# Optimization experiments

Hardware: AMD Instinct MI355X
Metric: run time of the kernel (lower is better)

The kernel has to match this reference:

```python
import jax, jax.numpy as jnp
import numpy as np

N = 50000      # nodes
E = 800000     # edges (before self-loops)
IN = 128
OUT = 128
HID = 2 * OUT  # hi=2 in the module
NEG_SLOPE = 0.2


def setup_inputs() -> dict:
    key = jax.random.key(0)
    ks = jax.random.split(key, 12)
    glorot = lambda k, shape: jax.random.normal(k, shape, jnp.float32) * (2.0 / (shape[0] + shape[-1])) ** 0.5
    return {
        "x": jax.random.normal(ks[0], (N, IN), jnp.float32),
        "edge_index": jax.random.randint(ks[1], (2, E), 0, N, jnp.int64),
        # layer 1: in -> 2*out
        "W1": glorot(ks[2], (IN, HID)),
        "a1_src": glorot(ks[3], (HID,)),
        "a1_dst": glorot(ks[4], (HID,)),
        "b1": jnp.zeros((HID,), jnp.float32),
        # layer 2: 2*out -> out
        "W2": glorot(ks[5], (HID, OUT)),
        "a2_src": glorot(ks[6], (OUT,)),
        "a2_dst": glorot(ks[7], (OUT,)),
        "b2": jnp.zeros((OUT,), jnp.float32),
    }


def gat_layer(x, src, dst, W, a_src, a_dst, b, n):
    # h = W x   [N, F]
    h = x @ W
    alpha_src = h @ a_src  # [N]
    alpha_dst = h @ a_dst  # [N]
    # per-edge attention logit, edge j->i uses src score of j + dst score of i
    e = jax.nn.leaky_relu(alpha_src[src] + alpha_dst[dst], NEG_SLOPE)  # [E']
    # numerically stable segment softmax over incoming edges of each dst node
    e_max = jax.lax.stop_gradient(jax.ops.segment_max(e, dst, num_segments=n))
    p = jnp.exp(e - e_max[dst])
    denom = jax.ops.segment_sum(p, dst, num_segments=n)
    alpha = p / (denom[dst] + 1e-16)  # [E']
    # weighted scatter-aggregate of source features
    out = jax.ops.segment_sum(h[src] * alpha[:, None], dst, num_segments=n)
    return out + b


def reference(x, edge_index, W1, a1_src, a1_dst, b1, W2, a2_src, a2_dst, b2):
    n = x.shape[0]
    loops = jnp.arange(n, dtype=edge_index.dtype)
    src = jnp.concatenate([edge_index[0], loops])  # add self-loops (PyG default)
    dst = jnp.concatenate([edge_index[1], loops])
    h = jax.nn.relu(gat_layer(x, src, dst, W1, a1_src, a1_dst, b1, n))
    out = jax.nn.relu(gat_layer(h, src, dst, W2, a2_src, a2_dst, b2, n))
    return out
```

## Files before the change

### kernel.cpp

```cpp
#include <hip/hip_runtime.h>
#include <hip/hip_bf16.h>
#include <float.h>
#include <stdint.h>

#define NEG_SLOPE 0.2f

typedef __attribute__((ext_vector_type(8))) short short8;
typedef __attribute__((ext_vector_type(4))) float f32x4;

#define BSTRIDE 3072

__device__ inline float b2f(unsigned short u) {
  return __uint_as_float((unsigned int)u << 16);
}
__device__ inline unsigned short f2b(float f) {
  unsigned int u = __float_as_uint(f);
  return (unsigned short)((u + 0x7FFF + ((u >> 16) & 1)) >> 16);
}
__device__ inline float leaky(float e) { return e >= 0.f ? e : NEG_SLOPE * e; }
__device__ inline float blo(unsigned int w) {
  return __uint_as_float(w << 16);
}
__device__ inline float bhi(unsigned int w) {
  return __uint_as_float(w & 0xFFFF0000u);
}

__global__ void detect_idx64_kernel(const void* ei, int* flag) {
  const int* p = (const int*)ei;
  int lane = threadIdx.x & 63;
  unsigned long long b = __ballot(p[2 * lane + 1] != 0);
  if (threadIdx.x == 0) *flag = (b == 0ull) ? 1 : 0;
}

__device__ inline int load_idx(const void* ei, long long pos, int is64) {
  if (is64) return (int)((const long long*)ei)[pos];
  return ((const int*)ei)[pos];
}

__global__ __launch_bounds__(256) void bin_edges(
    const void* __restrict__ ei, const int* __restrict__ flag64, int E,
    int* __restrict__ bcursor, unsigned int* __restrict__ binned) {
  __shared__ int hist[512];
  __shared__ int scn[512];
  __shared__ int gb[512];
  __shared__ unsigned int stage[2048];
  int t = threadIdx.x;
  hist[t] = 0; hist[t + 256] = 0;
  __syncthreads();
  const int is64 = *flag64;
  const long long base = (long long)blockIdx.x * 2048;
  const int cblk = (int)min((long long)2048, (long long)E - base);
  int sv[8];
  short bk[8], rk[8];
#pragma unroll
  for (int i = 0; i < 8; ++i) {
    int k = t + i * 256;
    if (k < cblk) {
      long long j = base + k;
      int s = load_idx(ei, j, is64);
      int d = load_idx(ei, (long long)E + j, is64);
      int b = d >> 7;
      bk[i] = (short)b;
      sv[i] = (s << 7) | (d & 127);
      rk[i] = (short)atomicAdd(&hist[b], 1);
    } else {
      bk[i] = -1;
    }
  }
  __syncthreads();
  scn[t] = hist[t]; scn[t + 256] = hist[t + 256];
  __syncthreads();
  for (int off = 1; off < 512; off <<= 1) {
    int v0 = (t >= off) ? scn[t - off] : 0;
    int v1 = scn[t + 256 - off];
    __syncthreads();
    scn[t] += v0;
    scn[t + 256] += v1;
    __syncthreads();
  }
  int c0 = hist[t], c1 = hist[t + 256];
  int l0 = scn[t] - c0, l1 = scn[t + 256] - c1;
  if (c0) gb[t] = atomicAdd(&bcursor[t], c0);
  if (c1) gb[t + 256] = atomicAdd(&bcursor[t + 256], c1);
  scn[t] = l0; scn[t + 256] = l1;
  __syncthreads();
#pragma unroll
  for (int i = 0; i < 8; ++i) {
    if (bk[i] >= 0)
      stage[scn[bk[i]] + rk[i]] = ((unsigned)(int)bk[i] << 23) | (unsigned)sv[i];
  }
  __syncthreads();
#pragma unroll
  for (int i = 0; i < 8; ++i) {
    int k = t + i * 256;
    if (k < cblk) {
      unsigned w = stage[k];
      int b = w >> 23;
      binned[(long long)b * BSTRIDE + gb[b] + (k - scn[b])] = w;
    }
  }
}

__global__ __launch_bounds__(256) void place_csr(
    const unsigned int* __restrict__ binned, const int* __restrict__ bcursor,
    int2* __restrict__ rowbe, unsigned short* __restrict__ csr, int Nn) {
  __shared__ int cnt[128], deg0[128], cur[128];
  int t = threadIdx.x;
  int b = blockIdx.x;
  if (t < 128) cnt[t] = 0;
  __syncthreads();
  const int rbeg = b * BSTRIDE;
  const int rend = rbeg + bcursor[b];
  for (int k = rbeg + t; k < rend; k += 256)
    atomicAdd(&cnt[binned[k] & 127], 1);
  __syncthreads();
  if (t < 128) deg0[t] = cnt[t];
  __syncthreads();
  for (int off = 1; off < 128; off <<= 1) {
    int v = (t >= off && t < 128) ? cnt[t - off] : 0;
    __syncthreads();
    if (t < 128) cnt[t] += v;
    __syncthreads();
  }
  const int node0 = b << 7;
  if (t < 128) {
    int start = rbeg + cnt[t] - deg0[t];
    int node = node0 + t;
    if (node < Nn) rowbe[node] = make_int2(start, start + deg0[t]);
    cur[t] = start;
  }
  __syncthreads();
  for (int k = rbeg + t; k < rend; k += 256) {
    unsigned w = binned[k];
    int pos = atomicAdd(&cur[w & 127], 1);
    csr[pos] = (unsigned short)((w >> 7) & 0xFFFF);
  }
}

__global__ __launch_bounds__(256) void prep_weights(
    const float* __restrict__ W1, const float* __restrict__ W2,
    const float* __restrict__ a1s, const float* __restrict__ a1d,
    const float* __restrict__ a2s, const float* __restrict__ a2d,
    unsigned short* __restrict__ Wp1, unsigned short* __restrict__ Wp2,
    float* __restrict__ wa) {
  int b = blockIdx.x;
  int t = threadIdx.x;
  if (b < 128) {
    int i = b * 256 + t;
    int k = i >> 8, n = i & 255;
    Wp1[(((k >> 3) * 256 + n) << 3) + (k & 7)] = f2b(W1[i]);
  } else if (b < 256) {
    int i = (b - 128) * 256 + t;
    int k = i >> 7, n = i & 127;
    Wp2[(((k >> 3) * 128 + n) << 3) + (k & 7)] = f2b(W2[i]);
  } else {
    int o = (b - 256) * 256 + t;
    float s = 0.f;
    if (o < 128) {
      for (int n = 0; n < 256; ++n) s += W1[o * 256 + n] * a1s[n];
    } else if (o < 256) {
      int k = o - 128;
      for (int n = 0; n < 256; ++n) s += W1[k * 256 + n] * a1d[n];
    } else if (o < 512) {
      int k = o - 256;
      for (int n = 0; n < 128; ++n) s += W2[k * 128 + n] * a2s[n];
    } else {
      int k = o - 512;
      for (int n = 0; n < 128; ++n) s += W2[k * 128 + n] * a2d[n];
    }
    wa[o] = s;
  }
}

__global__ __launch_bounds__(256) void alpha1_cast(
    const float* __restrict__ x, const float* __restrict__ wa,
    unsigned short* __restrict__ xb, float* __restrict__ as_out,
    float* __restrict__ ad_out, int Nn) {
  int node = blockIdx.x * 4 + (threadIdx.x >> 6);
  int lane = threadIdx.x & 63;
  if (node >= Nn) return;
  float2 v = *(const float2*)(x + (long long)node * 128 + lane * 2);
  float s1 = v.x * wa[lane * 2] + v.y * wa[lane * 2 + 1];
  float s2 = v.x * wa[128 + lane * 2] + v.y * wa[128 + lane * 2 + 1];
  unsigned int packed = (unsigned int)f2b(v.x) | ((unsigned int)f2b(v.y) << 16);
  *(unsigned int*)(xb + (long long)node * 128 + lane * 2) = packed;
#pragma unroll
  for (int off = 32; off > 0; off >>= 1) {
    s1 += __shfl_down(s1, off);
    s2 += __shfl_down(s2, off);
  }
  if (lane == 0) {
    as_out[node] = s1;
    ad_out[node] = s2;
  }
}

template <int Nn, int Kk, bool BIAS_RELU, bool SCORES>
__global__ __launch_bounds__(256) void gemm_mfma(
    const unsigned short* __restrict__ A, const unsigned short* __restrict__ Bp,
    unsigned short* __restrict__ C, int M, const float* __restrict__ bias,
    const float* __restrict__ was, const float* __restrict__ wad,
    float* __restrict__ s_as, float* __restrict__ s_ad) {
  const int l = threadIdx.x & 63;
  const int wm = threadIdx.x >> 6;
  const int bm = blockIdx.x * 64;
  const int bn = blockIdx.y * 64;
  const int arow = bm + wm * 16 + (l & 15);
  const int kg = l >> 4;

  f32x4 acc[4];
#pragma unroll
  for (int nt = 0; nt < 4; ++nt) acc[nt] = (f32x4){0.f, 0.f, 0.f, 0.f};

  const bool arow_ok = (arow < M);
  const bool do_scores = SCORES && (blockIdx.y == 0);
  float ps = 0.f, pd = 0.f;
#pragma unroll
  for (int kk = 0; kk < Kk; kk += 32) {
    short8 afrag;
    if (arow_ok)
      afrag = *(const short8*)(A + (long long)arow * Kk + kk + kg * 8);
    else
      afrag = (short8){0, 0, 0, 0, 0, 0, 0, 0};
    if (SCORES) {
      if (do_scores) {
        const int kb0 = kk + kg * 8;
#pragma unroll
        for (int i = 0; i < 8; ++i) {
          float v = b2f((unsigned short)afrag[i]);
          ps += v * was[kb0 + i];
          pd += v * wad[kb0 + i];
        }
      }
    }
    const int kb = (kk >> 3) + kg;
#pragma unroll
    for (int nt = 0; nt < 4; ++nt) {
      short8 bfrag = *(const short8*)(Bp + (((long long)kb * Nn + bn + nt * 16 +
                                             (l & 15))
                                            << 3));
      acc[nt] = __builtin_amdgcn_mfma_f32_16x16x32_bf16(afrag, bfrag, acc[nt],
                                                        0, 0, 0);
    }
  }
  if (SCORES) {
    if (do_scores) {
      ps += __shfl_xor(ps, 16); ps += __shfl_xor(ps, 32);
      pd += __shfl_xor(pd, 16); pd += __shfl_xor(pd, 32);
      if (l < 16 && arow_ok) {
        s_as[arow] = ps;
        s_ad[arow] = pd;
      }
    }
  }
#pragma unroll
  for (int nt = 0; nt < 4; ++nt) {
    const int col = bn + nt * 16 + (l & 15);
    float bv = BIAS_RELU ? bias[col] : 0.f;
#pragma unroll
    for (int r = 0; r < 4; ++r) {
      const int row = bm + wm * 16 + (l >> 4) * 4 + r;
      if (row < M) {
        float v = acc[nt][r];
        if (BIAS_RELU) v = fmaxf(v + bv, 0.f);
        C[(long long)row * Nn + col] = f2b(v);
      }
    }
  }
}

template <bool BIAS_RELU, bool OUT_BF16>
__global__ __launch_bounds__(256) void gat_aggregate(
    const int2* __restrict__ rowbe, const unsigned short* __restrict__ csr,
    const float* __restrict__ as, const float* __restrict__ ad,
    const unsigned short* __restrict__ h, const float* __restrict__ bias,
    void* __restrict__ outp, int Nn) {
  constexpr int F = 128;
  int node = blockIdx.x * 4 + (threadIdx.x >> 6);
  int lane = threadIdx.x & 63;
  if (node >= Nn) return;
  const int2 be = rowbe[node];
  const int beg = be.x, end = be.y;
  const int deg = end - beg;
  const float adn = ad[node];
  const int grp = lane >> 4;
  const int hl = lane & 15;
  const int f0 = hl * 8;

  const int chunk = (deg + 3) >> 2;
  int t = beg + grp * chunk;
  const int gend = min(t + chunk, end);

  float m, sg;
  float acc[8];
  if (grp == 0) {
    m = leaky(as[node] + adn);
    sg = 1.f;
    uint4 w = *(const uint4*)(h + (long long)node * F + f0);
    acc[0] = blo(w.x); acc[1] = bhi(w.x);
    acc[2] = blo(w.y); acc[3] = bhi(w.y);
    acc[4] = blo(w.z); acc[5] = bhi(w.z);
    acc[6] = blo(w.w); acc[7] = bhi(w.w);
  } else {
    m = -3.4e38f;
    sg = 0.f;
#pragma unroll
    for (int j = 0; j < 8; ++j) acc[j] = 0.f;
  }

  for (; t + 4 <= gend; t += 4) {
    int s0 = csr[t], s1 = csr[t + 1], s2 = csr[t + 2], s3 = csr[t + 3];
    uint4 w0 = *(const uint4*)(h + (long long)s0 * F + f0);
    uint4 w1 = *(const uint4*)(h + (long long)s1 * F + f0);
    uint4 w2 = *(const uint4*)(h + (long long)s2 * F + f0);
    uint4 w3 = *(const uint4*)(h + (long long)s3 * F + f0);
    float e0 = leaky(as[s0] + adn);
    float e1 = leaky(as[s1] + adn);
    float e2 = leaky(as[s2] + adn);
    float e3 = leaky(as[s3] + adn);
    float em = fmaxf(fmaxf(e0, e1), fmaxf(e2, e3));
    if (em > m + 8.f) {
      float sc = __expf(m - em);
      sg *= sc;
#pragma unroll
      for (int j = 0; j < 8; ++j) acc[j] *= sc;
      m = em;
    }
    float p0 = __expf(e0 - m), p1 = __expf(e1 - m);
    float p2 = __expf(e2 - m), p3 = __expf(e3 - m);
    sg += (p0 + p1) + (p2 + p3);
    acc[0] += p0 * blo(w0.x) + p1 * blo(w1.x) + p2 * blo(w2.x) + p3 * blo(w3.x);
    acc[1] += p0 * bhi(w0.x) + p1 * bhi(w1.x) + p2 * bhi(w2.x) + p3 * bhi(w3.x);
    acc[2] += p0 * blo(w0.y) + p1 * blo(w1.y) + p2 * blo(w2.y) + p3 * blo(w3.y);
    acc[3] += p0 * bhi(w0.y) + p1 * bhi(w1.y) + p2 * bhi(w2.y) + p3 * bhi(w3.y);
    acc[4] += p0 * blo(w0.z) + p1 * blo(w1.z) + p2 * blo(w2.z) + p3 * blo(w3.z);
    acc[5] += p0 * bhi(w0.z) + p1 * bhi(w1.z) + p2 * bhi(w2.z) + p3 * bhi(w3.z);
    acc[6] += p0 * blo(w0.w) + p1 * blo(w1.w) + p2 * blo(w2.w) + p3 * blo(w3.w);
    acc[7] += p0 * bhi(w0.w) + p1 * bhi(w1.w) + p2 * bhi(w2.w) + p3 * bhi(w3.w);
  }
  for (; t < gend; ++t) {
    int s = csr[t];
    uint4 w = *(const uint4*)(h + (long long)s * F + f0);
    float e = leaky(as[s] + adn);
    if (e > m + 8.f) {
      float sc = __expf(m - e);
      sg *= sc;
#pragma unroll
      for (int j = 0; j < 8; ++j) acc[j] *= sc;
      m = e;
    }
    float p = __expf(e - m);
    sg += p;
    acc[0] += p * blo(w.x); acc[1] += p * bhi(w.x);
    acc[2] += p * blo(w.y); acc[3] += p * bhi(w.y);
    acc[4] += p * blo(w.z); acc[5] += p * bhi(w.z);
    acc[6] += p * blo(w.w); acc[7] += p * bhi(w.w);
  }

#pragma unroll
  for (int off = 16; off <= 32; off <<= 1) {
    float mo = __shfl_xor(m, off);
    float so = __shfl_xor(sg, off);
    float mn = fmaxf(m, mo);
    float c0 = __expf(m - mn);
    float c1 = __expf(mo - mn);
    sg = sg * c0 + so * c1;
#pragma unroll
    for (int j = 0; j < 8; ++j) {
      float ao = __shfl_xor(acc[j], off);
      acc[j] = acc[j] * c0 + ao * c1;
    }
    m = mn;
  }
  const float inv = 1.f / (sg + 1e-16f);

  if (lane < 16) {
#pragma unroll
    for (int j = 0; j < 8; ++j) {
      acc[j] *= inv;
      if (BIAS_RELU) acc[j] = fmaxf(acc[j] + bias[f0 + j], 0.f);
    }
    if (OUT_BF16) {
      short8 o;
#pragma unroll
      for (int j = 0; j < 8; ++j) o[j] = (short)f2b(acc[j]);
      *(short8*)((unsigned short*)outp + (long long)node * F + f0) = o;
    } else {
      float4 o0 = {acc[0], acc[1], acc[2], acc[3]};
      float4 o1 = {acc[4], acc[5], acc[6], acc[7]};
      float* orow = (float*)outp + (long long)node * F + f0;
      *(float4*)(orow) = o0;
      *(float4*)(orow + 4) = o1;
    }
  }
}

extern "C" void kernel_launch(void* const* d_in, const int* in_sizes, int n_in,
                              void* d_out, int out_size, void* d_ws,
                              size_t ws_size, hipStream_t stream) {
  const float* x      = (const float*)d_in[0];
  const void*  ei     = d_in[1];
  const float* W1     = (const float*)d_in[2];
  const float* a1_src = (const float*)d_in[3];
  const float* a1_dst = (const float*)d_in[4];
  const float* b1     = (const float*)d_in[5];
  const float* W2     = (const float*)d_in[6];
  const float* a2_src = (const float*)d_in[7];
  const float* a2_dst = (const float*)d_in[8];
  const float* b2     = (const float*)d_in[9];
  float* out = (float*)d_out;

  const int N = 50000, E = 800000, IN = 128, HID = 256, OUT = 128;
  const int NBLK_E = (E + 2047) / 2048;
  const int NB = (N + 127) >> 7;

  char* ws = (char*)d_ws;
  size_t off = 0;
  auto carve = [&](size_t bytes) -> void* {
    void* p = ws + off;
    off = (off + bytes + 255) & ~(size_t)255;
    return p;
  };
  unsigned short* xb     = (unsigned short*)carve((size_t)N * IN * 2);
  unsigned short* aggx   = (unsigned short*)carve((size_t)N * IN * 2);
  unsigned short* out1   = (unsigned short*)carve((size_t)N * HID * 2);
  unsigned short* h2     = (unsigned short*)carve((size_t)N * OUT * 2);
  unsigned short* Wp1    = (unsigned short*)carve((size_t)IN * HID * 2);
  unsigned short* Wp2    = (unsigned short*)carve((size_t)HID * OUT * 2);
  float*          wa     = (float*)carve(768 * 4);
  unsigned int*   binned = (unsigned int*)carve((size_t)NB * BSTRIDE * 4);
  unsigned short* csr    = (unsigned short*)carve((size_t)NB * BSTRIDE * 2);
  int*            bcur   = (int*)carve(512 * 4);
  int2*           rowbe  = (int2*)carve((size_t)N * 8);
  float*          as_    = (float*)carve((size_t)N * 4);
  float*          ad_    = (float*)carve((size_t)N * 4);
  float*          as2_   = (float*)carve((size_t)N * 4);
  float*          ad2_   = (float*)carve((size_t)N * 4);
  int*            flag64 = (int*)carve(256);
  (void)ws_size; (void)in_sizes; (void)n_in; (void)out_size;

  hipMemsetAsync(bcur, 0, 512 * 4, stream);
  detect_idx64_kernel<<<1, 64, 0, stream>>>(ei, flag64);

  bin_edges<<<NBLK_E, 256, 0, stream>>>(ei, flag64, E, bcur, binned);
  place_csr<<<NB, 256, 0, stream>>>(binned, bcur, rowbe, csr, N);

  prep_weights<<<259, 256, 0, stream>>>(W1, W2, a1_src, a1_dst, a2_src, a2_dst,
                                        Wp1, Wp2, wa);

  const int nb4 = (N + 3) / 4;

  alpha1_cast<<<nb4, 256, 0, stream>>>(x, wa, xb, as_, ad_, N);
  gat_aggregate<false, true><<<nb4, 256, 0, stream>>>(rowbe, csr, as_, ad_,
                                                      xb, nullptr, aggx, N);
  {
    dim3 g((N + 63) / 64, HID / 64);
    gemm_mfma<HID, IN, true, false><<<g, 256, 0, stream>>>(
        aggx, Wp1, out1, N, b1, nullptr, nullptr, nullptr, nullptr);
  }

  {
    dim3 g((N + 63) / 64, OUT / 64);
    gemm_mfma<OUT, HID, false, true><<<g, 256, 0, stream>>>(
        out1, Wp2, h2, N, nullptr, wa + 256, wa + 512, as2_, ad2_);
  }
  gat_aggregate<true, false><<<nb4, 256, 0, stream>>>(rowbe, csr, as2_,
                                                      ad2_, h2, b2, out, N);
}
```

Baseline: 171.9 us.

## Use one 16-lane group per node in aggregation and merge setup kernels

The aggregation kernel now gives each node a 16-lane group that walks the whole edge list, where before a full wavefront split the edges into four chunks and merged the partial softmax state with cross-lane shuffles. This removes the shuffle merge and the idle lanes at the store, and puts four times as many nodes in each block. The trade-off is less parallelism per node, so high-degree nodes form longer serial chains. Separately, the memset and the index-width detection kernel are folded into the weight-prep kernel, which cuts launch overhead.

```diff
diff --git a/kernel.cpp b/kernel.cpp
--- a/kernel.cpp
+++ b/kernel.cpp
@@ -25,124 +25,18 @@
   return __uint_as_float(w & 0xFFFF0000u);
 }
 
-__global__ void detect_idx64_kernel(const void* ei, int* flag) {
-  const int* p = (const int*)ei;
-  int lane = threadIdx.x & 63;
-  unsigned long long b = __ballot(p[2 * lane + 1] != 0);
-  if (threadIdx.x == 0) *flag = (b == 0ull) ? 1 : 0;
-}
-
 __device__ inline int load_idx(const void* ei, long long pos, int is64) {
   if (is64) return (int)((const long long*)ei)[pos];
   return ((const int*)ei)[pos];
 }
 
-__global__ __launch_bounds__(256) void bin_edges(
-    const void* __restrict__ ei, const int* __restrict__ flag64, int E,
-    int* __restrict__ bcursor, unsigned int* __restrict__ binned) {
-  __shared__ int hist[512];
-  __shared__ int scn[512];
-  __shared__ int gb[512];
-  __shared__ unsigned int stage[2048];
-  int t = threadIdx.x;
-  hist[t] = 0; hist[t + 256] = 0;
-  __syncthreads();
-  const int is64 = *flag64;
-  const long long base = (long long)blockIdx.x * 2048;
-  const int cblk = (int)min((long long)2048, (long long)E - base);
-  int sv[8];
-  short bk[8], rk[8];
-#pragma unroll
-  for (int i = 0; i < 8; ++i) {
-    int k = t + i * 256;
-    if (k < cblk) {
-      long long j = base + k;
-      int s = load_idx(ei, j, is64);
-      int d = load_idx(ei, (long long)E + j, is64);
-      int b = d >> 7;
-      bk[i] = (short)b;
-      sv[i] = (s << 7) | (d & 127);
-      rk[i] = (short)atomicAdd(&hist[b], 1);
-    } else {
-      bk[i] = -1;
-    }
-  }
-  __syncthreads();
-  scn[t] = hist[t]; scn[t + 256] = hist[t + 256];
-  __syncthreads();
-  for (int off = 1; off < 512; off <<= 1) {
-    int v0 = (t >= off) ? scn[t - off] : 0;
-    int v1 = scn[t + 256 - off];
-    __syncthreads();
-    scn[t] += v0;
-    scn[t + 256] += v1;
-    __syncthreads();
-  }
-  int c0 = hist[t], c1 = hist[t + 256];
-  int l0 = scn[t] - c0, l1 = scn[t + 256] - c1;
-  if (c0) gb[t] = atomicAdd(&bcursor[t], c0);
-  if (c1) gb[t + 256] = atomicAdd(&bcursor[t + 256], c1);
-  scn[t] = l0; scn[t + 256] = l1;
-  __syncthreads();
-#pragma unroll
-  for (int i = 0; i < 8; ++i) {
-    if (bk[i] >= 0)
-      stage[scn[bk[i]] + rk[i]] = ((unsigned)(int)bk[i] << 23) | (unsigned)sv[i];
-  }
-  __syncthreads();
-#pragma unroll
-  for (int i = 0; i < 8; ++i) {
-    int k = t + i * 256;
-    if (k < cblk) {
-      unsigned w = stage[k];
-      int b = w >> 23;
-      binned[(long long)b * BSTRIDE + gb[b] + (k - scn[b])] = w;
-    }
-  }
-}
-
-__global__ __launch_bounds__(256) void place_csr(
-    const unsigned int* __restrict__ binned, const int* __restrict__ bcursor,
-    int2* __restrict__ rowbe, unsigned short* __restrict__ csr, int Nn) {
-  __shared__ int cnt[128], deg0[128], cur[128];
-  int t = threadIdx.x;
-  int b = blockIdx.x;
-  if (t < 128) cnt[t] = 0;
-  __syncthreads();
-  const int rbeg = b * BSTRIDE;
-  const int rend = rbeg + bcursor[b];
-  for (int k = rbeg + t; k < rend; k += 256)
-    atomicAdd(&cnt[binned[k] & 127], 1);
-  __syncthreads();
-  if (t < 128) deg0[t] = cnt[t];
-  __syncthreads();
-  for (int off = 1; off < 128; off <<= 1) {
-    int v = (t >= off && t < 128) ? cnt[t - off] : 0;
-    __syncthreads();
-    if (t < 128) cnt[t] += v;
-    __syncthreads();
-  }
-  const int node0 = b << 7;
-  if (t < 128) {
-    int start = rbeg + cnt[t] - deg0[t];
-    int node = node0 + t;
-    if (node < Nn) rowbe[node] = make_int2(start, start + deg0[t]);
-    cur[t] = start;
-  }
-  __syncthreads();
-  for (int k = rbeg + t; k < rend; k += 256) {
-    unsigned w = binned[k];
-    int pos = atomicAdd(&cur[w & 127], 1);
-    csr[pos] = (unsigned short)((w >> 7) & 0xFFFF);
-  }
-}
-
-__global__ __launch_bounds__(256) void prep_weights(
+__global__ __launch_bounds__(256) void prep_all(
     const float* __restrict__ W1, const float* __restrict__ W2,
     const float* __restrict__ a1s, const float* __restrict__ a1d,
     const float* __restrict__ a2s, const float* __restrict__ a2d,
     unsigned short* __restrict__ Wp1, unsigned short* __restrict__ Wp2,
-    float* __restrict__ wa) {
+    float* __restrict__ wa, int* __restrict__ bcur, const void* __restrict__ ei,
+    int* __restrict__ flag64) {
   int b = blockIdx.x;
   int t = threadIdx.x;
   if (b < 128) {
@@ -153,7 +47,7 @@
     int i = (b - 128) * 256 + t;
     int k = i >> 7, n = i & 127;
     Wp2[(((k >> 3) * 128 + n) << 3) + (k & 7)] = f2b(W2[i]);
-  } else {
+  } else if (b < 259) {
     int o = (b - 256) * 256 + t;
     float s = 0.f;
     if (o < 128) {
@@ -169,6 +63,114 @@
       for (int n = 0; n < 128; ++n) s += W2[k * 128 + n] * a2d[n];
     }
     wa[o] = s;
+  } else {
+    bcur[t] = 0;
+    bcur[t + 256] = 0;
+    if (t < 64) {
+      const int* p = (const int*)ei;
+      unsigned long long bl = __ballot(p[2 * t + 1] != 0);
+      if (t == 0) *flag64 = (bl == 0ull) ? 1 : 0;
+    }
+  }
+}
+
+__global__ __launch_bounds__(256) void bin_edges(
+    const void* __restrict__ ei, const int* __restrict__ flag64, int E,
+    int* __restrict__ bcursor, unsigned int* __restrict__ binned) {
+  __shared__ int hist[512];
+  __shared__ int scn[512];
+  __shared__ int gb[512];
+  __shared__ unsigned int stage[2048];
+  int t = threadIdx.x;
+  hist[t] = 0; hist[t + 256] = 0;
+  __syncthreads();
+  const int is64 = *flag64;
+  const long long base = (long long)blockIdx.x * 2048;
+  const int cblk = (int)min((long long)2048, (long long)E - base);
+  int sv[8];
+  short bk[8], rk[8];
+#pragma unroll
+  for (int i = 0; i < 8; ++i) {
+    int k = t + i * 256;
+    if (k < cblk) {
+      long long j = base + k;
+      int s = load_idx(ei, j, is64);
+      int d = load_idx(ei, (long long)E + j, is64);
+      int b = d >> 7;
+      bk[i] = (short)b;
+      sv[i] = (s << 7) | (d & 127);
+      rk[i] = (short)atomicAdd(&hist[b], 1);
+    } else {
+      bk[i] = -1;
+    }
+  }
+  __syncthreads();
+  scn[t] = hist[t]; scn[t + 256] = hist[t + 256];
+  __syncthreads();
+  for (int off = 1; off < 512; off <<= 1) {
+    int v0 = (t >= off) ? scn[t - off] : 0;
+    int v1 = scn[t + 256 - off];
+    __syncthreads();
+    scn[t] += v0;
+    scn[t + 256] += v1;
+    __syncthreads();
+  }
+  int c0 = hist[t], c1 = hist[t + 256];
+  int l0 = scn[t] - c0, l1 = scn[t + 256] - c1;
+  if (c0) gb[t] = atomicAdd(&bcursor[t], c0);
+  if (c1) gb[t + 256] = atomicAdd(&bcursor[t + 256], c1);
+  scn[t] = l0; scn[t + 256] = l1;
+  __syncthreads();
+#pragma unroll
+  for (int i = 0; i < 8; ++i) {
+    if (bk[i] >= 0)
+      stage[scn[bk[i]] + rk[i]] = ((unsigned)(int)bk[i] << 23) | (unsigned)sv[i];
+  }
+  __syncthreads();
+#pragma unroll
+  for (int i = 0; i < 8; ++i) {
+    int k = t + i * 256;
+    if (k < cblk) {
+      unsigned w = stage[k];
+      int b = w >> 23;
+      binned[(long long)b * BSTRIDE + gb[b] + (k - scn[b])] = w;
+    }
+  }
+}
+
+__global__ __launch_bounds__(256) void place_csr(
+    const unsigned int* __restrict__ binned, const int* __restrict__ bcursor,
+    int2* __restrict__ rowbe, unsigned short* __restrict__ csr, int Nn) {
+  __shared__ int cnt[128], deg0[128], cur[128];
+  int t = threadIdx.x;
+  int b = blockIdx.x;
+  if (t < 128) cnt[t] = 0;
+  __syncthreads();
+  const int rbeg = b * BSTRIDE;
+  const int rend = rbeg + bcursor[b];
+  for (int k = rbeg + t; k < rend; k += 256)
+    atomicAdd(&cnt[binned[k] & 127], 1);
+  __syncthreads();
+  if (t < 128) deg0[t] = cnt[t];
+  __syncthreads();
+  for (int off = 1; off < 128; off <<= 1) {
+    int v = (t >= off && t < 128) ? cnt[t - off] : 0;
+    __syncthreads();
+    if (t < 128) cnt[t] += v;
+    __syncthreads();
+  }
+  const int node0 = b << 7;
+  if (t < 128) {
+    int start = rbeg + cnt[t] - deg0[t];
+    int node = node0 + t;
+    if (node < Nn) rowbe[node] = make_int2(start, start + deg0[t]);
+    cur[t] = start;
+  }
+  __syncthreads();
+  for (int k = rbeg + t; k < rend; k += 256) {
+    unsigned w = binned[k];
+    int pos = atomicAdd(&cur[w & 127], 1);
+    csr[pos] = (unsigned short)((w >> 7) & 0xFFFF);
   }
 }
 
@@ -276,39 +278,27 @@
     const unsigned short* __restrict__ h, const float* __restrict__ bias,
     void* __restrict__ outp, int Nn) {
   constexpr int F = 128;
-  int node = blockIdx.x * 4 + (threadIdx.x >> 6);
-  int lane = threadIdx.x & 63;
+  const int node = blockIdx.x * 16 + (threadIdx.x >> 4);
+  const int hl = threadIdx.x & 15;
   if (node >= Nn) return;
   const int2 be = rowbe[node];
-  const int beg = be.x, end = be.y;
-  const int deg = end - beg;
+  int t = be.x;
+  const int end = be.y;
   const float adn = ad[node];
-  const int grp = lane >> 4;
-  const int hl = lane & 15;
   const int f0 = hl * 8;
 
-  const int chunk = (deg + 3) >> 2;
-  int t = beg + grp * chunk;
-  const int gend = min(t + chunk, end);
-
-  float m, sg;
+  float m = leaky(as[node] + adn);
+  float sg = 1.f;
   float acc[8];
-  if (grp == 0) {
-    m = leaky(as[node] + adn);
-    sg = 1.f;
+  {
     uint4 w = *(const uint4*)(h + (long long)node * F + f0);
     acc[0] = blo(w.x); acc[1] = bhi(w.x);
     acc[2] = blo(w.y); acc[3] = bhi(w.y);
     acc[4] = blo(w.z); acc[5] = bhi(w.z);
     acc[6] = blo(w.w); acc[7] = bhi(w.w);
-  } else {
-    m = -3.4e38f;
-    sg = 0.f;
-#pragma unroll
-    for (int j = 0; j < 8; ++j) acc[j] = 0.f;
-  }
-
-  for (; t + 4 <= gend; t += 4) {
+  }
+
+  for (; t + 4 <= end; t += 4) {
     int s0 = csr[t], s1 = csr[t + 1], s2 = csr[t + 2], s3 = csr[t + 3];
     uint4 w0 = *(const uint4*)(h + (long long)s0 * F + f0);
     uint4 w1 = *(const uint4*)(h + (long long)s1 * F + f0);
@@ -338,7 +328,7 @@
     acc[6] += p0 * blo(w0.w) + p1 * blo(w1.w) + p2 * blo(w2.w) + p3 * blo(w3.w);
     acc[7] += p0 * bhi(w0.w) + p1 * bhi(w1.w) + p2 * bhi(w2.w) + p3 * bhi(w3.w);
   }
-  for (; t < gend; ++t) {
+  for (; t < end; ++t) {
     int s = csr[t];
     uint4 w = *(const uint4*)(h + (long long)s * F + f0);
     float e = leaky(as[s] + adn);
@@ -357,41 +347,23 @@
     acc[6] += p * blo(w.w); acc[7] += p * bhi(w.w);
   }
 
-#pragma unroll
-  for (int off = 16; off <= 32; off <<= 1) {
-    float mo = __shfl_xor(m, off);
-    float so = __shfl_xor(sg, off);
-    float mn = fmaxf(m, mo);
-    float c0 = __expf(m - mn);
-    float c1 = __expf(mo - mn);
-    sg = sg * c0 + so * c1;
-#pragma unroll
-    for (int j = 0; j < 8; ++j) {
-      float ao = __shfl_xor(acc[j], off);
-      acc[j] = acc[j] * c0 + ao * c1;
-    }
-    m = mn;
-  }
   const float inv = 1.f / (sg + 1e-16f);
-
-  if (lane < 16) {
-#pragma unroll
-    for (int j = 0; j < 8; ++j) {
-      acc[j] *= inv;
-      if (BIAS_RELU) acc[j] = fmaxf(acc[j] + bias[f0 + j], 0.f);
-    }
-    if (OUT_BF16) {
-      short8 o;
-#pragma unroll
-      for (int j = 0; j < 8; ++j) o[j] = (short)f2b(acc[j]);
-      *(short8*)((unsigned short*)outp + (long long)node * F + f0) = o;
-    } else {
-      float4 o0 = {acc[0], acc[1], acc[2], acc[3]};
-      float4 o1 = {acc[4], acc[5], acc[6], acc[7]};
-      float* orow = (float*)outp + (long long)node * F + f0;
-      *(float4*)(orow) = o0;
-      *(float4*)(orow + 4) = o1;
-    }
+#pragma unroll
+  for (int j = 0; j < 8; ++j) {
+    acc[j] *= inv;
+    if (BIAS_RELU) acc[j] = fmaxf(acc[j] + bias[f0 + j], 0.f);
+  }
+  if (OUT_BF16) {
+    short8 o;
+#pragma unroll
+    for (int j = 0; j < 8; ++j) o[j] = (short)f2b(acc[j]);
+    *(short8*)((unsigned short*)outp + (long long)node * F + f0) = o;
+  } else {
+    float4 o0 = {acc[0], acc[1], acc[2], acc[3]};
+    float4 o1 = {acc[4], acc[5], acc[6], acc[7]};
+    float* orow = (float*)outp + (long long)node * F + f0;
+    *(float4*)(orow) = o0;
+    *(float4*)(orow + 4) = o1;
   }
 }
 
@@ -439,20 +411,18 @@
   int*            flag64 = (int*)carve(256);
   (void)ws_size; (void)in_sizes; (void)n_in; (void)out_size;
 
-  hipMemsetAsync(bcur, 0, 512 * 4, stream);
-  detect_idx64_kernel<<<1, 64, 0, stream>>>(ei, flag64);
+  prep_all<<<260, 256, 0, stream>>>(W1, W2, a1_src, a1_dst, a2_src, a2_dst,
+                                    Wp1, Wp2, wa, bcur, ei, flag64);
 
   bin_edges<<<NBLK_E, 256, 0, stream>>>(ei, flag64, E, bcur, binned);
   place_csr<<<NB, 256, 0, stream>>>(binned, bcur, rowbe, csr, N);
 
-  prep_weights<<<259, 256, 0, stream>>>(W1, W2, a1_src, a1_dst, a2_src, a2_dst,
-                                        Wp1, Wp2, wa);
-
   const int nb4 = (N + 3) / 4;
+  const int nb16 = (N + 15) / 16;
 
   alpha1_cast<<<nb4, 256, 0, stream>>>(x, wa, xb, as_, ad_, N);
-  gat_aggregate<false, true><<<nb4, 256, 0, stream>>>(rowbe, csr, as_, ad_,
-                                                      xb, nullptr, aggx, N);
+  gat_aggregate<false, true><<<nb16, 256, 0, stream>>>(rowbe, csr, as_, ad_,
+                                                       xb, nullptr, aggx, N);
   {
     dim3 g((N + 63) / 64, HID / 64);
     gemm_mfma<HID, IN, true, false><<<g, 256, 0, stream>>>(
@@ -464,6 +434,6 @@
     gemm_mfma<OUT, HID, false, true><<<g, 256, 0, stream>>>(
         out1, Wp2, h2, N, nullptr, wa + 256, wa + 512, as2_, ad2_);
   }
-  gat_aggregate<true, false><<<nb4, 256, 0, stream>>>(rowbe, csr, as2_,
-                                                      ad2_, h2, b2, out, N);
-}
+  gat_aggregate<true, false><<<nb16, 256, 0, stream>>>(rowbe, csr, as2_,
+                                                       ad2_, h2, b2, out, N);
+}
```

After: 154.7 us. 10.0% less time.
